# Performance work log

Measured on AMD Instinct MI355X. Metric: run time of the kernel, lower is better.

## Reference

```python
import jax, jax.numpy as jnp
import numpy as np

N = 100000   # nodes
E = 3200000  # edges (avg degree 32)
F = 128      # node_features
H = 128      # GCN hidden
A = 1024     # num_actions
B = 256      # graphs in batch


def setup_inputs() -> dict:
    key = jax.random.key(0)
    ks = jax.random.split(key, 11)
    glorot = lambda k, shp: (jax.random.normal(k, shp, jnp.float32)
                             / np.sqrt(float(shp[0])))
    return {
        "x": jax.random.normal(ks[0], (N, F), jnp.float32),
        "edge_index": jax.random.randint(ks[1], (2, E), 0, N, dtype=jnp.int64),
        "batch": jnp.sort(jax.random.randint(ks[2], (N,), 0, B, dtype=jnp.int64)),
        "W1": glorot(ks[3], (F, H)), "b1": jnp.zeros((H,), jnp.float32),
        "W2": glorot(ks[4], (H, H)), "b2": jnp.zeros((H,), jnp.float32),
        "Wv": glorot(ks[5], (H, 1)), "bv": jnp.zeros((1,), jnp.float32),
        "Wp": glorot(ks[6], (H, A)), "bp": jnp.zeros((A,), jnp.float32),
    }


def reference(x, edge_index, batch, W1, b1, W2, b2, Wv, bv, Wp, bp):
    # --- GCN normalization (PyG gcn_norm with self-loops) ---
    loops = jnp.arange(N, dtype=edge_index.dtype)
    src = jnp.concatenate([edge_index[0], loops])  # [E+N] message sources
    dst = jnp.concatenate([edge_index[1], loops])  # [E+N] aggregation targets
    deg = jax.ops.segment_sum(jnp.ones(src.shape, jnp.float32), dst,
                              num_segments=N)       # in-degree incl. self-loop
    dinv = jax.lax.rsqrt(deg)                       # deg >= 1 due to self-loops
    norm = (dinv[src] * dinv[dst])[:, None]         # [E+N, 1]

    def gcn_conv(h, W, b):
        h = h @ W                                   # transform first (small GEMM)
        agg = jax.ops.segment_sum(h[src] * norm, dst, num_segments=N)
        return agg + b

    h = jax.nn.relu(gcn_conv(x, W1, b1))
    h = jax.nn.relu(gcn_conv(h, W2, b2))

    # --- global_mean_pool over graph ids ---
    counts = jax.ops.segment_sum(jnp.ones((N,), jnp.float32), batch,
                                 num_segments=B)
    pooled = jax.ops.segment_sum(h, batch, num_segments=B) \
             / jnp.maximum(counts, 1.0)[:, None]    # [B, H]

    v = jnp.tanh(pooled @ Wv + bv)                  # [B, 1]
    p = jax.nn.softmax(pooled @ Wp + bp, axis=-1)   # [B, A]
    return (v, p)
```

## Files before the change

kernel.cpp:

```cpp
#include <hip/hip_runtime.h>
#include <hip/hip_bf16.h>

#define GN 100000
#define GE 3200000
#define GH 128
#define GA 1024
#define GB 256

#define NBUK 391
#define BCAP 12288
#define B1BLK 5120
#define NBIN1 625

typedef __attribute__((ext_vector_type(8))) short short8v;
typedef __attribute__((ext_vector_type(4))) float f32x4v;

__device__ __forceinline__ unsigned int f2bf(float f) {
    unsigned int u = __float_as_uint(f);
    return (u + 0x7fffu + ((u >> 16) & 1u)) >> 16;
}
__device__ __forceinline__ float bflo(unsigned int u) { return __uint_as_float(u << 16); }
__device__ __forceinline__ float bfhi(unsigned int u) { return __uint_as_float(u & 0xffff0000u); }

__device__ __forceinline__ int wswz(int k, int n) {
    return (((k >> 5) * 8 + (n >> 4)) * 64 + ((k >> 3) & 3) * 16 + (n & 15)) * 8 + (k & 7);
}

__global__ __launch_bounds__(256) void k_prep(const float* __restrict__ W1,
                                              const float* __restrict__ W2,
                                              unsigned short* __restrict__ Wsw1,
                                              unsigned short* __restrict__ Wsw2,
                                              int* __restrict__ gcur) {
    int b = blockIdx.x, t = threadIdx.x;
    if (b < 64) {
        int idx = b * 256 + t;
        int k = idx >> 7, n = idx & 127;
        Wsw1[wswz(k, n)] = (unsigned short)f2bf(W1[idx]);
    } else if (b < 128) {
        int idx = (b - 64) * 256 + t;
        int k = idx >> 7, n = idx & 127;
        Wsw2[wswz(k, n)] = (unsigned short)f2bf(W2[idx]);
    } else {
        for (int i = t; i < NBUK; i += 256) gcur[i] = i * BCAP;
    }
}

__global__ __launch_bounds__(256) void k_bin1(const int* __restrict__ src,
                                              const int* __restrict__ dst,
                                              int* __restrict__ gcur,
                                              unsigned int* __restrict__ binned) {
    __shared__ int hist[512], lstart[512];
    __shared__ int curl[NBUK], gbase[NBUK];
    __shared__ unsigned int srec[B1BLK];
    __shared__ unsigned short sbuk[B1BLK];
    __shared__ int wsc[4];
    int t = threadIdx.x;
    hist[t] = 0; hist[t + 256] = 0;
    __syncthreads();
    int beg = blockIdx.x * B1BLK;
    unsigned int rec[20]; int bukv[20];
#pragma unroll
    for (int q = 0; q < 5; q++) {
        int4 s4 = *(const int4*)&src[beg + 4 * (t + 256 * q)];
        int4 d4 = *(const int4*)&dst[beg + 4 * (t + 256 * q)];
        int ss[4] = {s4.x, s4.y, s4.z, s4.w};
        int dd[4] = {d4.x, d4.y, d4.z, d4.w};
#pragma unroll
        for (int j = 0; j < 4; j++) {
            int k = q * 4 + j;
            rec[k] = (unsigned int)ss[j] | ((unsigned int)(dd[j] & 255) << 17);
            bukv[k] = dd[j] >> 8;
            atomicAdd(&hist[bukv[k]], 1);
        }
    }
    __syncthreads();
    int v0 = hist[2 * t], v1 = hist[2 * t + 1];
    int s = v0 + v1;
    int lane = t & 63, w = t >> 6;
    int x = s;
#pragma unroll
    for (int off = 1; off < 64; off <<= 1) {
        int y = __shfl_up(x, off);
        if (lane >= off) x += y;
    }
    if (lane == 63) wsc[w] = x;
    __syncthreads();
    int wo = 0;
#pragma unroll
    for (int i = 0; i < 4; i++)
        if (i < w) wo += wsc[i];
    int excl = wo + x - s;
    lstart[2 * t] = excl;
    lstart[2 * t + 1] = excl + v0;
    __syncthreads();
    for (int i = t; i < NBUK; i += 256) {
        curl[i] = lstart[i];
        int c = hist[i];
        gbase[i] = c ? atomicAdd(&gcur[i], c) : 0;
    }
    __syncthreads();
#pragma unroll
    for (int k = 0; k < 20; k++) {
        int p = atomicAdd(&curl[bukv[k]], 1);
        srec[p] = rec[k];
        sbuk[p] = (unsigned short)bukv[k];
    }
    __syncthreads();
    for (int i = t; i < B1BLK; i += 256) {
        int b = sbuk[i];
        binned[gbase[b] + (i - lstart[b])] = srec[i];
    }
}

__global__ __launch_bounds__(256) void k_sort2(const unsigned int* __restrict__ binned,
                                               const int* __restrict__ gcur,
                                               int* __restrict__ csr_src,
                                               int* __restrict__ nbeg,
                                               int* __restrict__ nend,
                                               float* __restrict__ dinv) {
    int b = blockIdx.x, t = threadIdx.x;
    __shared__ int hist[256], cur[256], wsum[4];
    hist[t] = 0;
    __syncthreads();
    int rbase = b * BCAP;
    int rend = gcur[b];
    int cnt = rend - rbase;
    int n4 = cnt >> 2;
    for (int i = t; i < n4; i += 256) {
        uint4 v = *(const uint4*)&binned[rbase + i * 4];
        atomicAdd(&hist[(v.x >> 17) & 255], 1);
        atomicAdd(&hist[(v.y >> 17) & 255], 1);
        atomicAdd(&hist[(v.z >> 17) & 255], 1);
        atomicAdd(&hist[(v.w >> 17) & 255], 1);
    }
    for (int e = rbase + n4 * 4 + t; e < rend; e += 256)
        atomicAdd(&hist[(binned[e] >> 17) & 255], 1);
    __syncthreads();
    int h = hist[t];
    int lane = t & 63, w = t >> 6;
    int x = h;
#pragma unroll
    for (int off = 1; off < 64; off <<= 1) {
        int y = __shfl_up(x, off);
        if (lane >= off) x += y;
    }
    if (lane == 63) wsum[w] = x;
    __syncthreads();
    int wo = 0;
#pragma unroll
    for (int i = 0; i < 4; i++)
        if (i < w) wo += wsum[i];
    int excl = wo + x - h;
    int node = (b << 8) + t;
    if (node < GN) {
        nbeg[node] = rbase + excl;
        nend[node] = rbase + excl + h;
        dinv[node] = rsqrtf((float)(h + 1));
    }
    cur[t] = excl;
    __syncthreads();
    for (int i = t; i < n4; i += 256) {
        uint4 v = *(const uint4*)&binned[rbase + i * 4];
        unsigned int vv[4] = {v.x, v.y, v.z, v.w};
#pragma unroll
        for (int j = 0; j < 4; j++) {
            int p = atomicAdd(&cur[(vv[j] >> 17) & 255], 1);
            csr_src[rbase + p] = (int)(vv[j] & 0x1FFFF);
        }
    }
    for (int e = rbase + n4 * 4 + t; e < rend; e += 256) {
        unsigned int v = binned[e];
        int p = atomicAdd(&cur[(v >> 17) & 255], 1);
        csr_src[rbase + p] = (int)(v & 0x1FFFF);
    }
}

__global__ __launch_bounds__(256) void k_gemm1(const float* __restrict__ A,
                                               const unsigned short* __restrict__ Wsw,
                                               const float* __restrict__ dinv,
                                               unsigned int* __restrict__ C) {
    __shared__ float Ct[64][128];
    int t = threadIdx.x;
    int row0 = blockIdx.x * 64;
    int wv = t >> 6, lane = t & 63;
    int m16 = lane & 15, g = lane >> 4;
    f32x4v acc[8];
#pragma unroll
    for (int nb = 0; nb < 8; nb++) acc[nb] = (f32x4v){0.f, 0.f, 0.f, 0.f};
    int arow = row0 + wv * 16 + m16; if (arow >= GN) arow = GN - 1;
#pragma unroll
    for (int kb = 0; kb < 4; kb++) {
        const float* ap = &A[(size_t)arow * 128 + kb * 32 + g * 8];
        float4 a0 = *(const float4*)ap;
        float4 a1 = *(const float4*)(ap + 4);
        uint4 up;
        up.x = f2bf(a0.x) | (f2bf(a0.y) << 16);
        up.y = f2bf(a0.z) | (f2bf(a0.w) << 16);
        up.z = f2bf(a1.x) | (f2bf(a1.y) << 16);
        up.w = f2bf(a1.z) | (f2bf(a1.w) << 16);
        short8v af = *(short8v*)&up;
#pragma unroll
        for (int nb = 0; nb < 8; nb++) {
            short8v bf = *(const short8v*)&Wsw[((kb * 8 + nb) * 64 + lane) * 8];
            acc[nb] = __builtin_amdgcn_mfma_f32_16x16x32_bf16(af, bf, acc[nb], 0, 0, 0);
        }
    }
#pragma unroll
    for (int nb = 0; nb < 8; nb++)
#pragma unroll
        for (int r = 0; r < 4; r++)
            Ct[wv * 16 + g * 4 + r][nb * 16 + m16] = acc[nb][r];
    __syncthreads();
    int lr = t >> 2, ch = t & 3;
    int grow = row0 + lr;
    if (grow < GN) {
        float dv = dinv[grow];
#pragma unroll
        for (int q = 0; q < 4; q++) {
            int c0 = ch * 32 + q * 8;
            uint4 po;
            po.x = f2bf(Ct[lr][c0 + 0] * dv) | (f2bf(Ct[lr][c0 + 1] * dv) << 16);
            po.y = f2bf(Ct[lr][c0 + 2] * dv) | (f2bf(Ct[lr][c0 + 3] * dv) << 16);
            po.z = f2bf(Ct[lr][c0 + 4] * dv) | (f2bf(Ct[lr][c0 + 5] * dv) << 16);
            po.w = f2bf(Ct[lr][c0 + 6] * dv) | (f2bf(Ct[lr][c0 + 7] * dv) << 16);
            *(uint4*)&C[(size_t)grow * 64 + ch * 16 + q * 4] = po;
        }
    }
}

__global__ __launch_bounds__(256) void k_gemm2(const unsigned int* __restrict__ A,
                                               const unsigned short* __restrict__ Wsw,
                                               const float* __restrict__ dinv,
                                               unsigned int* __restrict__ C) {
    __shared__ float Ct[64][128];
    int t = threadIdx.x;
    int row0 = blockIdx.x * 64;
    int wv = t >> 6, lane = t & 63;
    int m16 = lane & 15, g = lane >> 4;
    f32x4v acc[8];
#pragma unroll
    for (int nb = 0; nb < 8; nb++) acc[nb] = (f32x4v){0.f, 0.f, 0.f, 0.f};
    int arow = row0 + wv * 16 + m16; if (arow >= GN) arow = GN - 1;
#pragma unroll
    for (int kb = 0; kb < 4; kb++) {
        uint4 av = *(const uint4*)&A[(size_t)arow * 64 + kb * 16 + g * 4];
        short8v af = *(short8v*)&av;
#pragma unroll
        for (int nb = 0; nb < 8; nb++) {
            short8v bf = *(const short8v*)&Wsw[((kb * 8 + nb) * 64 + lane) * 8];
            acc[nb] = __builtin_amdgcn_mfma_f32_16x16x32_bf16(af, bf, acc[nb], 0, 0, 0);
        }
    }
#pragma unroll
    for (int nb = 0; nb < 8; nb++)
#pragma unroll
        for (int r = 0; r < 4; r++)
            Ct[wv * 16 + g * 4 + r][nb * 16 + m16] = acc[nb][r];
    __syncthreads();
    int lr = t >> 2, ch = t & 3;
    int grow = row0 + lr;
    if (grow < GN) {
        float dv = dinv[grow];
#pragma unroll
        for (int q = 0; q < 4; q++) {
            int c0 = ch * 32 + q * 8;
            uint4 po;
            po.x = f2bf(Ct[lr][c0 + 0] * dv) | (f2bf(Ct[lr][c0 + 1] * dv) << 16);
            po.y = f2bf(Ct[lr][c0 + 2] * dv) | (f2bf(Ct[lr][c0 + 3] * dv) << 16);
            po.z = f2bf(Ct[lr][c0 + 4] * dv) | (f2bf(Ct[lr][c0 + 5] * dv) << 16);
            po.w = f2bf(Ct[lr][c0 + 6] * dv) | (f2bf(Ct[lr][c0 + 7] * dv) << 16);
            *(uint4*)&C[(size_t)grow * 64 + ch * 16 + q * 4] = po;
        }
    }
}

__global__ __launch_bounds__(256) void k_aggregate(const unsigned int* __restrict__ ts,
                                                   const int* __restrict__ nbeg,
                                                   const int* __restrict__ nend,
                                                   const int* __restrict__ csr_src,
                                                   const float* __restrict__ dinv,
                                                   const float* __restrict__ bias,
                                                   unsigned int* __restrict__ out) {
    int node = blockIdx.x * 4 + (threadIdx.x >> 6);
    if (node >= GN) return;
    int lane = threadIdx.x & 63;
    int beg = nbeg[node];
    int end = nend[node];
    float di = dinv[node];
    float ax = 0.f, ay = 0.f;
    for (int base = beg; base < end; base += 64) {
        int n = end - base; if (n > 64) n = 64;
        int myidx = (lane < n) ? csr_src[base + lane] : 0;
        int k = 0;
        for (; k + 16 <= n; k += 16) {
            unsigned int u[16];
#pragma unroll
            for (int q = 0; q < 16; q++) {
                int s = __shfl(myidx, k + q);
                u[q] = ts[s * 64 + lane];
            }
#pragma unroll
            for (int q = 0; q < 16; q++) { ax += bflo(u[q]); ay += bfhi(u[q]); }
        }
        for (; k + 4 <= n; k += 4) {
            unsigned int u[4];
#pragma unroll
            for (int q = 0; q < 4; q++) {
                int s = __shfl(myidx, k + q);
                u[q] = ts[s * 64 + lane];
            }
#pragma unroll
            for (int q = 0; q < 4; q++) { ax += bflo(u[q]); ay += bfhi(u[q]); }
        }
        for (; k < n; k++) {
            int s = __shfl(myidx, k);
            unsigned int u = ts[s * 64 + lane];
            ax += bflo(u); ay += bfhi(u);
        }
    }
    unsigned int su = ts[(size_t)node * 64 + lane];
    float bx = bias[lane * 2 + 0], by = bias[lane * 2 + 1];
    float ox = fmaxf(fmaf(di, ax + bflo(su), bx), 0.f);
    float oy = fmaxf(fmaf(di, ay + bfhi(su), by), 0.f);
    out[(size_t)node * 64 + lane] = f2bf(ox) | (f2bf(oy) << 16);
}

__global__ __launch_bounds__(256) void k_pool(const unsigned int* __restrict__ h,
                                              const int* __restrict__ batch,
                                              float* __restrict__ pooled) {
    int g = blockIdx.x;
    int t = threadIdx.x;
    int f = t & 63, part = t >> 6;
    int lo = 0, hi = GN;
    while (lo < hi) { int m = (lo + hi) >> 1; if (batch[m] < g) lo = m + 1; else hi = m; }
    int start = lo;
    hi = GN;
    while (lo < hi) { int m = (lo + hi) >> 1; if (batch[m] <= g) lo = m + 1; else hi = m; }
    int end = lo;
    float ax = 0.f, ay = 0.f;
    for (int i = start + part; i < end; i += 4) {
        unsigned int u = h[(size_t)i * 64 + f];
        ax += bflo(u); ay += bfhi(u);
    }
    __shared__ float redx[256], redy[256];
    redx[t] = ax; redy[t] = ay;
    __syncthreads();
    if (part == 0) {
        float sx = redx[f] + redx[f + 64] + redx[f + 128] + redx[f + 192];
        float sy = redy[f] + redy[f + 64] + redy[f + 128] + redy[f + 192];
        float inv = 1.0f / fmaxf((float)(end - start), 1.0f);
        pooled[g * 128 + 2 * f + 0] = sx * inv;
        pooled[g * 128 + 2 * f + 1] = sy * inv;
    }
}

__global__ __launch_bounds__(256) void k_policy(const float* __restrict__ pooled,
                                                const float* __restrict__ Wp,
                                                const float* __restrict__ bp,
                                                const float* __restrict__ Wv,
                                                const float* __restrict__ bv,
                                                float* __restrict__ outv,
                                                float* __restrict__ outp) {
    int g0 = blockIdx.x * 4;
    int t = threadIdx.x;
    __shared__ float pr[4][128];
    __shared__ float red[256];
    if (t < 128) {
#pragma unroll
        for (int gg = 0; gg < 4; gg++)
            pr[gg][t] = pooled[(size_t)(g0 + gg) * 128 + t];
    }
    __syncthreads();
    float wvt = (t < 128) ? Wv[t] : 0.f;
#pragma unroll
    for (int gg = 0; gg < 4; gg++) {
        red[t] = (t < 128) ? pr[gg][t] * wvt : 0.f;
        __syncthreads();
        for (int off = 64; off > 0; off >>= 1) {
            if (t < off) red[t] += red[t + off];
            __syncthreads();
        }
        if (t == 0) outv[g0 + gg] = tanhf(red[0] + bv[0]);
        __syncthreads();
    }
    float bb0 = bp[t], bb1 = bp[t + 256], bb2 = bp[t + 512], bb3 = bp[t + 768];
    float acc[4][4];
#pragma unroll
    for (int gg = 0; gg < 4; gg++) {
        acc[gg][0] = bb0; acc[gg][1] = bb1; acc[gg][2] = bb2; acc[gg][3] = bb3;
    }
    for (int k = 0; k < 128; k++) {
        const float* wr = Wp + (size_t)k * 1024;
        float w0 = wr[t], w1 = wr[t + 256], w2 = wr[t + 512], w3 = wr[t + 768];
#pragma unroll
        for (int gg = 0; gg < 4; gg++) {
            float pv = pr[gg][k];
            acc[gg][0] = fmaf(pv, w0, acc[gg][0]);
            acc[gg][1] = fmaf(pv, w1, acc[gg][1]);
            acc[gg][2] = fmaf(pv, w2, acc[gg][2]);
            acc[gg][3] = fmaf(pv, w3, acc[gg][3]);
        }
    }
#pragma unroll
    for (int gg = 0; gg < 4; gg++) {
        float m = fmaxf(fmaxf(acc[gg][0], acc[gg][1]), fmaxf(acc[gg][2], acc[gg][3]));
        red[t] = m;
        __syncthreads();
        for (int off = 128; off > 0; off >>= 1) {
            if (t < off) red[t] = fmaxf(red[t], red[t + off]);
            __syncthreads();
        }
        float mx = red[0];
        __syncthreads();
        float e0 = __expf(acc[gg][0] - mx), e1 = __expf(acc[gg][1] - mx);
        float e2 = __expf(acc[gg][2] - mx), e3 = __expf(acc[gg][3] - mx);
        red[t] = (e0 + e1) + (e2 + e3);
        __syncthreads();
        for (int off = 128; off > 0; off >>= 1) {
            if (t < off) red[t] += red[t + off];
            __syncthreads();
        }
        float inv = 1.0f / red[0];
        __syncthreads();
        size_t ob = (size_t)(g0 + gg) * 1024;
        outp[ob + t + 0]   = e0 * inv;
        outp[ob + t + 256] = e1 * inv;
        outp[ob + t + 512] = e2 * inv;
        outp[ob + t + 768] = e3 * inv;
    }
}

extern "C" void kernel_launch(void* const* d_in, const int* in_sizes, int n_in,
                              void* d_out, int out_size, void* d_ws, size_t ws_size,
                              hipStream_t stream) {
    const float* x    = (const float*)d_in[0];
    const int*   ei   = (const int*)d_in[1];
    const int*   srcA = ei;
    const int*   dstA = ei + GE;
    const int*   batch = (const int*)d_in[2];
    const float* W1 = (const float*)d_in[3];
    const float* b1 = (const float*)d_in[4];
    const float* W2 = (const float*)d_in[5];
    const float* b2 = (const float*)d_in[6];
    const float* Wv = (const float*)d_in[7];
    const float* bv = (const float*)d_in[8];
    const float* Wp = (const float*)d_in[9];
    const float* bp = (const float*)d_in[10];
    float* out = (float*)d_out;

    char* ws = (char*)d_ws;
    unsigned int* bufH = (unsigned int*)ws;  ws += (size_t)GN * 64 * 4;
    unsigned int* ts_bf = (unsigned int*)ws; ws += (size_t)GN * 64 * 4;
    float* pooled = (float*)ws;      ws += (size_t)GB * 128 * 4;
    float* dinv = (float*)ws;        ws += (size_t)100352 * 4;
    int*   nbeg = (int*)ws;          ws += (size_t)100352 * 4;
    int*   nend = (int*)ws;          ws += (size_t)100352 * 4;
    int*   csr_src = (int*)ws;       ws += (size_t)NBUK * BCAP * 4;
    int*   gcur = (int*)ws;          ws += 512 * 4;
    unsigned short* Wsw1 = (unsigned short*)ws; ws += 16384 * 2;
    unsigned short* Wsw2 = (unsigned short*)ws; ws += 16384 * 2;
    unsigned int* binned = ts_bf;

    k_prep<<<129, 256, 0, stream>>>(W1, W2, Wsw1, Wsw2, gcur);
    k_bin1<<<NBIN1, 256, 0, stream>>>(srcA, dstA, gcur, binned);
    k_sort2<<<NBUK, 256, 0, stream>>>(binned, gcur, csr_src, nbeg, nend, dinv);

    k_gemm1<<<(GN + 63) / 64, 256, 0, stream>>>(x, Wsw1, dinv, ts_bf);
    k_aggregate<<<GN / 4, 256, 0, stream>>>(ts_bf, nbeg, nend, csr_src, dinv, b1, bufH);

    k_gemm2<<<(GN + 63) / 64, 256, 0, stream>>>(bufH, Wsw2, dinv, ts_bf);
    k_aggregate<<<GN / 4, 256, 0, stream>>>(ts_bf, nbeg, nend, csr_src, dinv, b2, bufH);

    k_pool<<<GB, 256, 0, stream>>>(bufH, batch, pooled);
    k_policy<<<GB / 4, 256, 0, stream>>>(pooled, Wp, bp, Wv, bv, out, out + GB);
}
```

Before: 364.1 us.

## Fuse mean pooling into second aggregation via atomic accumulation

The second GCN aggregation no longer writes the hidden features; each node atomically adds its ReLU output into a per-graph fp32 sum. The separate pooling kernel is removed, and the policy kernel computes per-graph counts by binary search and scales the sums. Aggregation blocks grow to 8 nodes (512 threads). This avoids writing and re-reading the full hidden matrix, but issues millions of contended float atomics onto a small set of addresses, and the float accumulation order becomes nondeterministic.

```diff
diff --git a/kernel.cpp b/kernel.cpp
--- a/kernel.cpp
+++ b/kernel.cpp
@@ -30,7 +30,8 @@
                                               const float* __restrict__ W2,
                                               unsigned short* __restrict__ Wsw1,
                                               unsigned short* __restrict__ Wsw2,
-                                              int* __restrict__ gcur) {
+                                              int* __restrict__ gcur,
+                                              float* __restrict__ psum) {
     int b = blockIdx.x, t = threadIdx.x;
     if (b < 64) {
         int idx = b * 256 + t;
@@ -40,8 +41,11 @@
         int idx = (b - 64) * 256 + t;
         int k = idx >> 7, n = idx & 127;
         Wsw2[wswz(k, n)] = (unsigned short)f2bf(W2[idx]);
+    } else if (b == 128) {
+        for (int i = t; i < NBUK; i += 256) gcur[i] = i * BCAP;
     } else {
-        for (int i = t; i < NBUK; i += 256) gcur[i] = i * BCAP;
+        int i = (b - 129) * 1024 + t * 4;
+        *(float4*)&psum[i] = make_float4(0.f, 0.f, 0.f, 0.f);
     }
 }
 
@@ -274,14 +278,16 @@
     }
 }
 
-__global__ __launch_bounds__(256) void k_aggregate(const unsigned int* __restrict__ ts,
+__global__ __launch_bounds__(512) void k_aggregate(const unsigned int* __restrict__ ts,
                                                    const int* __restrict__ nbeg,
                                                    const int* __restrict__ nend,
                                                    const int* __restrict__ csr_src,
                                                    const float* __restrict__ dinv,
                                                    const float* __restrict__ bias,
-                                                   unsigned int* __restrict__ out) {
-    int node = blockIdx.x * 4 + (threadIdx.x >> 6);
+                                                   unsigned int* __restrict__ out,
+                                                   const int* __restrict__ batch,
+                                                   float* __restrict__ psum) {
+    int node = blockIdx.x * 8 + (threadIdx.x >> 6);
     if (node >= GN) return;
     int lane = threadIdx.x & 63;
     int beg = nbeg[node];
@@ -322,39 +328,17 @@
     float bx = bias[lane * 2 + 0], by = bias[lane * 2 + 1];
     float ox = fmaxf(fmaf(di, ax + bflo(su), bx), 0.f);
     float oy = fmaxf(fmaf(di, ay + bfhi(su), by), 0.f);
-    out[(size_t)node * 64 + lane] = f2bf(ox) | (f2bf(oy) << 16);
-}
-
-__global__ __launch_bounds__(256) void k_pool(const unsigned int* __restrict__ h,
-                                              const int* __restrict__ batch,
-                                              float* __restrict__ pooled) {
-    int g = blockIdx.x;
-    int t = threadIdx.x;
-    int f = t & 63, part = t >> 6;
-    int lo = 0, hi = GN;
-    while (lo < hi) { int m = (lo + hi) >> 1; if (batch[m] < g) lo = m + 1; else hi = m; }
-    int start = lo;
-    hi = GN;
-    while (lo < hi) { int m = (lo + hi) >> 1; if (batch[m] <= g) lo = m + 1; else hi = m; }
-    int end = lo;
-    float ax = 0.f, ay = 0.f;
-    for (int i = start + part; i < end; i += 4) {
-        unsigned int u = h[(size_t)i * 64 + f];
-        ax += bflo(u); ay += bfhi(u);
-    }
-    __shared__ float redx[256], redy[256];
-    redx[t] = ax; redy[t] = ay;
-    __syncthreads();
-    if (part == 0) {
-        float sx = redx[f] + redx[f + 64] + redx[f + 128] + redx[f + 192];
-        float sy = redy[f] + redy[f + 64] + redy[f + 128] + redy[f + 192];
-        float inv = 1.0f / fmaxf((float)(end - start), 1.0f);
-        pooled[g * 128 + 2 * f + 0] = sx * inv;
-        pooled[g * 128 + 2 * f + 1] = sy * inv;
-    }
-}
-
-__global__ __launch_bounds__(256) void k_policy(const float* __restrict__ pooled,
+    if (psum == nullptr) {
+        out[(size_t)node * 64 + lane] = f2bf(ox) | (f2bf(oy) << 16);
+    } else {
+        int g = batch[node];
+        atomicAdd(&psum[g * 128 + lane * 2 + 0], ox);
+        atomicAdd(&psum[g * 128 + lane * 2 + 1], oy);
+    }
+}
+
+__global__ __launch_bounds__(256) void k_policy(const float* __restrict__ psum,
+                                                const int* __restrict__ batch,
                                                 const float* __restrict__ Wp,
                                                 const float* __restrict__ bp,
                                                 const float* __restrict__ Wv,
@@ -365,10 +349,21 @@
     int t = threadIdx.x;
     __shared__ float pr[4][128];
     __shared__ float red[256];
+    __shared__ float invc[4];
+    if (t < 4) {
+        int g = g0 + t;
+        int lo = 0, hi = GN;
+        while (lo < hi) { int m = (lo + hi) >> 1; if (batch[m] < g) lo = m + 1; else hi = m; }
+        int start = lo;
+        hi = GN;
+        while (lo < hi) { int m = (lo + hi) >> 1; if (batch[m] <= g) lo = m + 1; else hi = m; }
+        invc[t] = 1.0f / fmaxf((float)(lo - start), 1.0f);
+    }
+    __syncthreads();
     if (t < 128) {
 #pragma unroll
         for (int gg = 0; gg < 4; gg++)
-            pr[gg][t] = pooled[(size_t)(g0 + gg) * 128 + t];
+            pr[gg][t] = psum[(size_t)(g0 + gg) * 128 + t] * invc[gg];
     }
     __syncthreads();
     float wvt = (t < 128) ? Wv[t] : 0.f;
@@ -451,7 +446,7 @@
     char* ws = (char*)d_ws;
     unsigned int* bufH = (unsigned int*)ws;  ws += (size_t)GN * 64 * 4;
     unsigned int* ts_bf = (unsigned int*)ws; ws += (size_t)GN * 64 * 4;
-    float* pooled = (float*)ws;      ws += (size_t)GB * 128 * 4;
+    float* psum = (float*)ws;        ws += (size_t)GB * 128 * 4;
     float* dinv = (float*)ws;        ws += (size_t)100352 * 4;
     int*   nbeg = (int*)ws;          ws += (size_t)100352 * 4;
     int*   nend = (int*)ws;          ws += (size_t)100352 * 4;
@@ -461,16 +456,17 @@
     unsigned short* Wsw2 = (unsigned short*)ws; ws += 16384 * 2;
     unsigned int* binned = ts_bf;
 
-    k_prep<<<129, 256, 0, stream>>>(W1, W2, Wsw1, Wsw2, gcur);
+    k_prep<<<161, 256, 0, stream>>>(W1, W2, Wsw1, Wsw2, gcur, psum);
     k_bin1<<<NBIN1, 256, 0, stream>>>(srcA, dstA, gcur, binned);
     k_sort2<<<NBUK, 256, 0, stream>>>(binned, gcur, csr_src, nbeg, nend, dinv);
 
     k_gemm1<<<(GN + 63) / 64, 256, 0, stream>>>(x, Wsw1, dinv, ts_bf);
-    k_aggregate<<<GN / 4, 256, 0, stream>>>(ts_bf, nbeg, nend, csr_src, dinv, b1, bufH);
+    k_aggregate<<<GN / 8, 512, 0, stream>>>(ts_bf, nbeg, nend, csr_src, dinv, b1,
+                                            bufH, batch, nullptr);
 
     k_gemm2<<<(GN + 63) / 64, 256, 0, stream>>>(bufH, Wsw2, dinv, ts_bf);
-    k_aggregate<<<GN / 4, 256, 0, stream>>>(ts_bf, nbeg, nend, csr_src, dinv, b2, bufH);
-
-    k_pool<<<GB, 256, 0, stream>>>(bufH, batch, pooled);
-    k_policy<<<GB / 4, 256, 0, stream>>>(pooled, Wp, bp, Wv, bv, out, out + GB);
-}
+    k_aggregate<<<GN / 8, 512, 0, stream>>>(ts_bf, nbeg, nend, csr_src, dinv, b2,
+                                            nullptr, batch, psum);
+
+    k_policy<<<GB / 4, 256, 0, stream>>>(psum, batch, Wp, bp, Wv, bv, out, out + GB);
+}
```

Result: slower. 418.4 us (+14.9%).
